# Kernel optimization log

Hardware: AMD Instinct MI355X
Metric: run time of the kernel (lower is better)

Reference implementation:

```python
import jax, jax.numpy as jnp
import numpy as np
import math

NEG = -9e15
NOISE_SCALE = 0.4

def _gat(h, A, a0, a1, a2, a3):
    # e_k[b,i,j] = leakyrelu(sum_d h[b,i,d]*h[b,j,d]*a_k[d])  (== (h[i]*h[j]) @ a_k)
    def score(a):
        return jax.nn.leaky_relu(jnp.einsum('bid,bjd->bij', h * a, h), 0.2)
    e0, e1, e2, e3 = score(a0), score(a1), score(a2), score(a3)
    alpha = jnp.where(A == 1, e0, NEG)
    alpha = jnp.where(A == 2, e1, alpha)
    alpha = jnp.where(A == 3, e2, alpha)
    alpha = jnp.where(A == 4, e3, alpha)
    alpha = jax.nn.softmax(alpha, axis=-1)
    return jnp.einsum('bij,bjd->bid', alpha, h)

def _ave_pooling(h, mask):
    length = jnp.sum(mask, axis=1)                      # [B]
    return jnp.sum(h * mask[:, :, None], axis=1) / length[:, None]

def _att_pooling(h, star, mask):
    sim = jnp.exp(jnp.einsum('bnd,bd->bn', h, star))    # [B,N]
    sim = sim * mask
    sim = sim / (jnp.sum(sim, axis=-1, keepdims=True) + 1e-24)
    return jnp.sum(sim[:, :, None] * h, axis=1)         # [B,D]

def _forward(A, hidden, graph_mask, a0, a1, a2, a3, noise):
    step, D = noise.shape[0], hidden.shape[-1]
    star = _ave_pooling(hidden, graph_mask)
    embs = []
    for i in range(step):
        hidden = _gat(hidden, A, a0, a1, a2, a3)
        sim = jnp.einsum('bnd,bd->bn', hidden, star) / math.sqrt(D)
        alpha = jax.nn.sigmoid(sim)[:, :, None]
        hidden = (1.0 - alpha) * hidden + alpha * star[:, None, :]
        n = noise[i]
        n = n / jnp.maximum(jnp.linalg.norm(n, axis=-1, keepdims=True), 1e-12)
        hidden = hidden + jnp.sign(hidden) * n * NOISE_SCALE
        star = _att_pooling(hidden, star, graph_mask)
        embs.append(hidden)
    embeddings_cl = jnp.mean(jnp.stack(embs, axis=1), axis=1)
    return hidden, star, embeddings_cl

def setup_inputs() -> dict:
    key = jax.random.key(0)
    ks = jax.random.split(key, 8)
    B, N, D, STEP = 256, 128, 512, 3
    A = jax.random.randint(ks[0], (B, N, N), 0, 5, dtype=jnp.int64)
    hidden = jax.random.normal(ks[1], (B, N, D), dtype=jnp.float32)
    graph_mask = jnp.ones((B, N), dtype=jnp.float32)
    a0 = jax.random.normal(ks[2], (D,), dtype=jnp.float32) * 0.1
    a1 = jax.random.normal(ks[3], (D,), dtype=jnp.float32) * 0.1
    a2 = jax.random.normal(ks[4], (D,), dtype=jnp.float32) * 0.1
    a3 = jax.random.normal(ks[5], (D,), dtype=jnp.float32) * 0.1
    noise = jax.random.uniform(ks[6], (STEP, B, N, D), dtype=jnp.float32)
    return {"A": A, "hidden": hidden, "graph_mask": graph_mask,
            "a0": a0, "a1": a1, "a2": a2, "a3": a3, "noise": noise}

def reference(A, hidden, graph_mask, a0, a1, a2, a3, noise):
    return _forward(A, hidden, graph_mask, a0, a1, a2, a3, noise)
```

## Files before the change

kernel.cpp:

```cpp
#include <hip/hip_runtime.h>
#include <math.h>

#define BB 256
#define NN 128
#define DD 512
#define NEGV (-9e15f)

__global__ __launch_bounds__(256) void k_avepool(const float* __restrict__ h,
                                                 const float* __restrict__ mask,
                                                 float* __restrict__ star) {
    const int b = blockIdx.x;
    const int t = threadIdx.x;
    const float* hb = h + (size_t)b * NN * DD;
    const float* mb = mask + (size_t)b * NN;
    float acc0 = 0.f, acc1 = 0.f, L = 0.f;
    for (int n = 0; n < NN; ++n) {
        float m = mb[n];
        L += m;
        acc0 += m * hb[n * DD + t];
        acc1 += m * hb[n * DD + t + 256];
    }
    star[b * DD + t] = acc0 / L;
    star[b * DD + t + 256] = acc1 / L;
}

__global__ __launch_bounds__(1024, 1) void k_gat(const float* __restrict__ h_in,
                                                 const int* __restrict__ A,
                                                 const float* __restrict__ a0,
                                                 const float* __restrict__ a1,
                                                 const float* __restrict__ a2,
                                                 const float* __restrict__ a3,
                                                 float* __restrict__ h_gat) {
    __shared__ float4 hA[NN * 17];
    __shared__ float4 hB[NN * 17];
    __shared__ float  eselS[NN * 132];

    const int tid = threadIdx.x;
    const int b = blockIdx.x;
    const float* __restrict__ hb = h_in + (size_t)b * NN * DD;

    const bool fullJob = tid < 512;
    const bool quarterJob = (tid >= 512) && (tid < 768);
    int jjb = 0, jr = 0;
    if (fullJob) {
        int rem = tid;
        for (int k = 0; k < 16; ++k) {
            int c = 4 * k + 4;
            if (rem < c) { jjb = k; jr = rem; break; }
            rem -= c;
        }
    }
    const int i0 = jr * 2, i1 = i0 + 1;
    const int jb8 = jjb * 8;
    const int swi = (jr >> 2) & 7;
    const int swj = jjb & 7;
    const int qi = tid - 512;
    const int qrow = 64 + (qi >> 2);
    const int qj0 = 120 + 2 * (qi & 3);
    const int qswi = (qrow >> 3) & 7;

    auto stageAll = [&](float4* buf, int d0) {
        #pragma unroll
        for (int q = 0; q < 2; ++q) {
            int l = q * 1024 + tid;
            int row = l >> 4, c4 = l & 15;
            buf[row * 17 + (c4 ^ ((row >> 3) & 7))] = *(const float4*)(hb + row * DD + d0 + c4 * 4);
        }
    };

    float acc0[8][4], acc1[8][4];
    #pragma unroll
    for (int jj = 0; jj < 8; ++jj)
        #pragma unroll
        for (int k = 0; k < 4; ++k) { acc0[jj][k] = 0.f; acc1[jj][k] = 0.f; }

    stageAll(hA, 0);
    __syncthreads();
    for (int ck = 0; ck < 8; ++ck) {
        const int d0 = ck * 64;
        const float4* cur = (ck & 1) ? hB : hA;
        float4* nxt = (ck & 1) ? hA : hB;
        if (ck < 7) stageAll(nxt, d0 + 64);
        if (fullJob) {
            #pragma unroll 2
            for (int c4 = 0; c4 < 16; ++c4) {
                const int dbase = d0 + c4 * 4;
                const float av0x = a0[dbase],     av0y = a1[dbase],     av0z = a2[dbase],     av0w = a3[dbase];
                const float av1x = a0[dbase + 1], av1y = a1[dbase + 1], av1z = a2[dbase + 1], av1w = a3[dbase + 1];
                const float av2x = a0[dbase + 2], av2y = a1[dbase + 2], av2z = a2[dbase + 2], av2w = a3[dbase + 2];
                const float av3x = a0[dbase + 3], av3y = a1[dbase + 3], av3z = a2[dbase + 3], av3w = a3[dbase + 3];
                float4 hi0 = cur[i0 * 17 + (c4 ^ swi)];
                float4 hi1 = cur[i1 * 17 + (c4 ^ swi)];
                #pragma unroll
                for (int jj = 0; jj < 8; ++jj) {
                    float4 hj = cur[(jb8 + jj) * 17 + (c4 ^ swj)];
                    float p;
                    p = hi0.x * hj.x; acc0[jj][0] += p * av0x; acc0[jj][1] += p * av0y; acc0[jj][2] += p * av0z; acc0[jj][3] += p * av0w;
                    p = hi0.y * hj.y; acc0[jj][0] += p * av1x; acc0[jj][1] += p * av1y; acc0[jj][2] += p * av1z; acc0[jj][3] += p * av1w;
                    p = hi0.z * hj.z; acc0[jj][0] += p * av2x; acc0[jj][1] += p * av2y; acc0[jj][2] += p * av2z; acc0[jj][3] += p * av2w;
                    p = hi0.w * hj.w; acc0[jj][0] += p * av3x; acc0[jj][1] += p * av3y; acc0[jj][2] += p * av3z; acc0[jj][3] += p * av3w;
                    p = hi1.x * hj.x; acc1[jj][0] += p * av0x; acc1[jj][1] += p * av0y; acc1[jj][2] += p * av0z; acc1[jj][3] += p * av0w;
                    p = hi1.y * hj.y; acc1[jj][0] += p * av1x; acc1[jj][1] += p * av1y; acc1[jj][2] += p * av1z; acc1[jj][3] += p * av1w;
                    p = hi1.z * hj.z; acc1[jj][0] += p * av2x; acc1[jj][1] += p * av2y; acc1[jj][2] += p * av2z; acc1[jj][3] += p * av2w;
                    p = hi1.w * hj.w; acc1[jj][0] += p * av3x; acc1[jj][1] += p * av3y; acc1[jj][2] += p * av3z; acc1[jj][3] += p * av3w;
                }
            }
        } else if (quarterJob) {
            #pragma unroll 2
            for (int c4 = 0; c4 < 16; ++c4) {
                const int dbase = d0 + c4 * 4;
                const float av0x = a0[dbase],     av0y = a1[dbase],     av0z = a2[dbase],     av0w = a3[dbase];
                const float av1x = a0[dbase + 1], av1y = a1[dbase + 1], av1z = a2[dbase + 1], av1w = a3[dbase + 1];
                const float av2x = a0[dbase + 2], av2y = a1[dbase + 2], av2z = a2[dbase + 2], av2w = a3[dbase + 2];
                const float av3x = a0[dbase + 3], av3y = a1[dbase + 3], av3z = a2[dbase + 3], av3w = a3[dbase + 3];
                float4 hi0 = cur[qrow * 17 + (c4 ^ qswi)];
                #pragma unroll
                for (int jj = 0; jj < 2; ++jj) {
                    float4 hj = cur[(qj0 + jj) * 17 + (c4 ^ 7)];
                    float p;
                    p = hi0.x * hj.x; acc0[jj][0] += p * av0x; acc0[jj][1] += p * av0y; acc0[jj][2] += p * av0z; acc0[jj][3] += p * av0w;
                    p = hi0.y * hj.y; acc0[jj][0] += p * av1x; acc0[jj][1] += p * av1y; acc0[jj][2] += p * av1z; acc0[jj][3] += p * av1w;
                    p = hi0.z * hj.z; acc0[jj][0] += p * av2x; acc0[jj][1] += p * av2y; acc0[jj][2] += p * av2z; acc0[jj][3] += p * av2w;
                    p = hi0.w * hj.w; acc0[jj][0] += p * av3x; acc0[jj][1] += p * av3y; acc0[jj][2] += p * av3z; acc0[jj][3] += p * av3w;
                }
            }
        }
        __syncthreads();
    }

    {
        auto selv = [](const float* a4, int Av) -> float {
            float e = (Av == 1) ? a4[0] : (Av == 2) ? a4[1] : (Av == 3) ? a4[2] : a4[3];
            float lr = (e > 0.f) ? e : 0.2f * e;
            return (Av >= 1 && Av <= 4) ? lr : NEGV;
        };
        const int* __restrict__ Ab = A + (size_t)b * NN * NN;
        if (fullJob) {
            #pragma unroll
            for (int jj = 0; jj < 8; ++jj) {
                const int j = jb8 + jj;
                int Av;
                Av = Ab[i0 * NN + j];  eselS[i0 * 132 + j] = selv(acc0[jj], Av);
                Av = Ab[i1 * NN + j];  eselS[i1 * 132 + j] = selv(acc1[jj], Av);
                Av = Ab[j * NN + i0];  eselS[j * 132 + i0] = selv(acc0[jj], Av);
                Av = Ab[j * NN + i1];  eselS[j * 132 + i1] = selv(acc1[jj], Av);
            }
        } else if (quarterJob) {
            #pragma unroll
            for (int jj = 0; jj < 2; ++jj) {
                const int j = qj0 + jj;
                int Av;
                Av = Ab[qrow * NN + j];  eselS[qrow * 132 + j] = selv(acc0[jj], Av);
                Av = Ab[j * NN + qrow];  eselS[j * 132 + qrow] = selv(acc0[jj], Av);
            }
        }
        __syncthreads();
    }

    {
        const int it4 = tid >> 8;
        const int sub = tid & 255;
        const int ti = sub >> 4, tj = sub & 15;
        const int li0 = it4 * 32 + ti * 2, li1 = li0 + 1;
        float s0[8], s1[8];
        #pragma unroll
        for (int jj = 0; jj < 8; ++jj) {
            s0[jj] = eselS[li0 * 132 + tj + 16 * jj];
            s1[jj] = eselS[li1 * 132 + tj + 16 * jj];
        }
        float m0 = s0[0], m1 = s1[0];
        #pragma unroll
        for (int jj = 1; jj < 8; ++jj) { m0 = fmaxf(m0, s0[jj]); m1 = fmaxf(m1, s1[jj]); }
        #pragma unroll
        for (int off = 1; off < 16; off <<= 1) {
            m0 = fmaxf(m0, __shfl_xor(m0, off));
            m1 = fmaxf(m1, __shfl_xor(m1, off));
        }
        float e0[8], e1[8], sum0 = 0.f, sum1 = 0.f;
        #pragma unroll
        for (int jj = 0; jj < 8; ++jj) {
            e0[jj] = expf(s0[jj] - m0); sum0 += e0[jj];
            e1[jj] = expf(s1[jj] - m1); sum1 += e1[jj];
        }
        #pragma unroll
        for (int off = 1; off < 16; off <<= 1) {
            sum0 += __shfl_xor(sum0, off);
            sum1 += __shfl_xor(sum1, off);
        }
        #pragma unroll
        for (int jj = 0; jj < 8; ++jj) {
            eselS[li0 * 132 + tj + 16 * jj] = e0[jj] / sum0;
            eselS[li1 * 132 + tj + 16 * jj] = e1[jj] / sum1;
        }
    }
    __syncthreads();

    stageAll(hA, 0);
    __syncthreads();
    const int gd = tid & 15, jh = (tid >> 4) & 1, rsub = (tid >> 5) & 1, wv = tid >> 6;
    const int rbase = wv * 16 + rsub;
    const int jbase = jh * 64;
#define PVROW(r, ac) { s[r].x += (ac) * hv.x; s[r].y += (ac) * hv.y; s[r].z += (ac) * hv.z; s[r].w += (ac) * hv.w; }
    for (int ck = 0; ck < 8; ++ck) {
        const int d0 = ck * 64;
        const float4* cur = (ck & 1) ? hB : hA;
        float4* nxt = (ck & 1) ? hA : hB;
        if (tid >= 512) {
            if (ck < 7) {
                #pragma unroll
                for (int q = 0; q < 4; ++q) {
                    int l = q * 512 + (tid - 512);
                    int row = l >> 4, c4 = l & 15;
                    nxt[row * 17 + (c4 ^ ((row >> 3) & 7))] = *(const float4*)(hb + row * DD + d0 + 64 + c4 * 4);
                }
            }
        } else {
            float4 s[8];
            #pragma unroll
            for (int r = 0; r < 8; ++r) s[r] = make_float4(0.f, 0.f, 0.f, 0.f);
            #pragma unroll 2
            for (int jq = 0; jq < 16; ++jq) {
                const int j0 = jbase + jq * 4;
                const int swz = (j0 >> 3) & 7;
                float4 av0 = *(const float4*)(&eselS[(rbase +  0) * 132 + j0]);
                float4 av1 = *(const float4*)(&eselS[(rbase +  2) * 132 + j0]);
                float4 av2 = *(const float4*)(&eselS[(rbase +  4) * 132 + j0]);
                float4 av3 = *(const float4*)(&eselS[(rbase +  6) * 132 + j0]);
                float4 av4 = *(const float4*)(&eselS[(rbase +  8) * 132 + j0]);
                float4 av5 = *(const float4*)(&eselS[(rbase + 10) * 132 + j0]);
                float4 av6 = *(const float4*)(&eselS[(rbase + 12) * 132 + j0]);
                float4 av7 = *(const float4*)(&eselS[(rbase + 14) * 132 + j0]);
                float4 hv;
                hv = cur[(j0 + 0) * 17 + (gd ^ swz)];
                PVROW(0, av0.x) PVROW(1, av1.x) PVROW(2, av2.x) PVROW(3, av3.x)
                PVROW(4, av4.x) PVROW(5, av5.x) PVROW(6, av6.x) PVROW(7, av7.x)
                hv = cur[(j0 + 1) * 17 + (gd ^ swz)];
                PVROW(0, av0.y) PVROW(1, av1.y) PVROW(2, av2.y) PVROW(3, av3.y)
                PVROW(4, av4.y) PVROW(5, av5.y) PVROW(6, av6.y) PVROW(7, av7.y)
                hv = cur[(j0 + 2) * 17 + (gd ^ swz)];
                PVROW(0, av0.z) PVROW(1, av1.z) PVROW(2, av2.z) PVROW(3, av3.z)
                PVROW(4, av4.z) PVROW(5, av5.z) PVROW(6, av6.z) PVROW(7, av7.z)
                hv = cur[(j0 + 3) * 17 + (gd ^ swz)];
                PVROW(0, av0.w) PVROW(1, av1.w) PVROW(2, av2.w) PVROW(3, av3.w)
                PVROW(4, av4.w) PVROW(5, av5.w) PVROW(6, av6.w) PVROW(7, av7.w)
            }
            #pragma unroll
            for (int r = 0; r < 8; ++r) {
                float mx = __shfl_xor(s[r].x, 16);
                float my = __shfl_xor(s[r].y, 16);
                float mz = __shfl_xor(s[r].z, 16);
                float mw = __shfl_xor(s[r].w, 16);
                s[r].x += mx; s[r].y += my; s[r].z += mz; s[r].w += mw;
            }
            if (jh == 0) {
                float* outp = h_gat + ((size_t)b * NN + rbase) * DD + d0 + gd * 4;
                #pragma unroll
                for (int r = 0; r < 8; ++r) *(float4*)(outp + (size_t)(2 * r) * DD) = s[r];
            }
        }
        __syncthreads();
    }
#undef PVROW
}

__global__ __launch_bounds__(256) void k_mix(const float* __restrict__ h_gat,
                                             const float* __restrict__ star,
                                             const float* __restrict__ noise_s,
                                             const float* __restrict__ h1p,
                                             const float* __restrict__ h2p,
                                             float* __restrict__ h_out,
                                             float* __restrict__ embs,
                                             float* __restrict__ sims,
                                             int mode) {
    const int b = blockIdx.y;
    const int tid = threadIdx.x;
    const int wave = tid >> 6, lane = tid & 63;
    const int row0 = blockIdx.x * 16 + wave * 4;
    const float* stp = star + (size_t)b * DD + lane * 8;
    float4 st0 = *(const float4*)(stp);
    float4 st1 = *(const float4*)(stp + 4);
    const float inv3 = 1.0f / 3.0f;

    for (int rr = 0; rr < 4; ++rr) {
        const int row = row0 + rr;
        const size_t base = ((size_t)b * NN + row) * DD + lane * 8;
        float4 hg0 = *(const float4*)(h_gat + base);
        float4 hg1 = *(const float4*)(h_gat + base + 4);
        float4 n0 = *(const float4*)(noise_s + base);
        float4 n1 = *(const float4*)(noise_s + base + 4);
        float dot = hg0.x*st0.x + hg0.y*st0.y + hg0.z*st0.z + hg0.w*st0.w
                  + hg1.x*st1.x + hg1.y*st1.y + hg1.z*st1.z + hg1.w*st1.w;
        float nn = n0.x*n0.x + n0.y*n0.y + n0.z*n0.z + n0.w*n0.w
                 + n1.x*n1.x + n1.y*n1.y + n1.z*n1.z + n1.w*n1.w;
        #pragma unroll
        for (int off = 1; off < 64; off <<= 1) {
            dot += __shfl_xor(dot, off);
            nn  += __shfl_xor(nn, off);
        }
        const float sim = dot / 22.62741699796952f;
        const float al = 1.0f / (1.0f + expf(-sim));
        const float ns = 0.4f / fmaxf(sqrtf(nn), 1e-12f);

        float hm, sg, hn[8];
        float hgv[8] = {hg0.x,hg0.y,hg0.z,hg0.w,hg1.x,hg1.y,hg1.z,hg1.w};
        float stv[8] = {st0.x,st0.y,st0.z,st0.w,st1.x,st1.y,st1.z,st1.w};
        float nv [8] = {n0.x,n0.y,n0.z,n0.w,n1.x,n1.y,n1.z,n1.w};
        #pragma unroll
        for (int c = 0; c < 8; ++c) {
            hm = (1.0f - al) * hgv[c] + al * stv[c];
            sg = (hm > 0.f) ? 1.f : ((hm < 0.f) ? -1.f : 0.f);
            hn[c] = hm + sg * nv[c] * ns;
        }
        *(float4*)(h_out + base)     = make_float4(hn[0], hn[1], hn[2], hn[3]);
        *(float4*)(h_out + base + 4) = make_float4(hn[4], hn[5], hn[6], hn[7]);

        float d2 = hn[0]*stv[0] + hn[1]*stv[1] + hn[2]*stv[2] + hn[3]*stv[3]
                 + hn[4]*stv[4] + hn[5]*stv[5] + hn[6]*stv[6] + hn[7]*stv[7];
        #pragma unroll
        for (int off = 1; off < 64; off <<= 1) d2 += __shfl_xor(d2, off);
        if (lane == 0) sims[b * NN + row] = d2;

        if (mode == 1) {
            float4 a0v = *(const float4*)(h1p + base);
            float4 a1v = *(const float4*)(h1p + base + 4);
            float4 b0v = *(const float4*)(h2p + base);
            float4 b1v = *(const float4*)(h2p + base + 4);
            float h1v[8] = {a0v.x,a0v.y,a0v.z,a0v.w,a1v.x,a1v.y,a1v.z,a1v.w};
            float h2v[8] = {b0v.x,b0v.y,b0v.z,b0v.w,b1v.x,b1v.y,b1v.z,b1v.w};
            float ev[8];
            #pragma unroll
            for (int c = 0; c < 8; ++c) {
                float e = h1v[c] * inv3;
                e += h2v[c] * inv3;
                e += hn[c] * inv3;
                ev[c] = e;
            }
            *(float4*)(embs + base)     = make_float4(ev[0], ev[1], ev[2], ev[3]);
            *(float4*)(embs + base + 4) = make_float4(ev[4], ev[5], ev[6], ev[7]);
        } else if (mode == 2) {
            *(float4*)(embs + base)     = make_float4(hn[0]*inv3, hn[1]*inv3, hn[2]*inv3, hn[3]*inv3);
            *(float4*)(embs + base + 4) = make_float4(hn[4]*inv3, hn[5]*inv3, hn[6]*inv3, hn[7]*inv3);
        } else if (mode == 3) {
            float4 ea = *(const float4*)(embs + base);
            float4 eb = *(const float4*)(embs + base + 4);
            ea.x += hn[0]*inv3; ea.y += hn[1]*inv3; ea.z += hn[2]*inv3; ea.w += hn[3]*inv3;
            eb.x += hn[4]*inv3; eb.y += hn[5]*inv3; eb.z += hn[6]*inv3; eb.w += hn[7]*inv3;
            *(float4*)(embs + base)     = ea;
            *(float4*)(embs + base + 4) = eb;
        }
    }
}

__global__ __launch_bounds__(256) void k_attpool2(const float* __restrict__ h,
                                                  const float* __restrict__ sims,
                                                  const float* __restrict__ mask,
                                                  float* __restrict__ star_out) {
    __shared__ float simS[NN];
    __shared__ float wS[NN];
    __shared__ float sh_M, sh_inv;
    const int b = blockIdx.x;
    const int tid = threadIdx.x;
    if (tid < NN) simS[tid] = sims[b * NN + tid];
    __syncthreads();
    if (tid < 64) {
        float v = fmaxf(simS[tid], simS[tid + 64]);
        #pragma unroll
        for (int off = 1; off < 64; off <<= 1) v = fmaxf(v, __shfl_xor(v, off));
        if (tid == 0) sh_M = v;
    }
    __syncthreads();
    const float M = sh_M;
    if (tid < NN) wS[tid] = expf(simS[tid] - M) * mask[b * NN + tid];
    __syncthreads();
    if (tid < 64) {
        float v = wS[tid] + wS[tid + 64];
        #pragma unroll
        for (int off = 1; off < 64; off <<= 1) v += __shfl_xor(v, off);
        if (tid == 0) sh_inv = 1.0f / (v + 1e-24f * expf(-M));
    }
    __syncthreads();
    const float inv = sh_inv;
    const float* hb = h + (size_t)b * NN * DD;
    float acc0 = 0.f, acc1 = 0.f;
    for (int n = 0; n < NN; ++n) {
        const float w = wS[n];
        acc0 += w * hb[n * DD + tid];
        acc1 += w * hb[n * DD + tid + 256];
    }
    star_out[b * DD + tid] = acc0 * inv;
    star_out[b * DD + tid + 256] = acc1 * inv;
}

extern "C" void kernel_launch(void* const* d_in, const int* in_sizes, int n_in,
                              void* d_out, int out_size, void* d_ws, size_t ws_size,
                              hipStream_t stream) {
    const int*   A      = (const int*)d_in[0];
    const float* hidden = (const float*)d_in[1];
    const float* mask   = (const float*)d_in[2];
    const float* a0     = (const float*)d_in[3];
    const float* a1     = (const float*)d_in[4];
    const float* a2     = (const float*)d_in[5];
    const float* a3     = (const float*)d_in[6];
    const float* noise  = (const float*)d_in[7];

    float* out_h    = (float*)d_out;
    float* out_star = out_h + (size_t)BB * NN * DD;
    float* out_embs = out_star + (size_t)BB * DD;

    const size_t hElems = (size_t)BB * NN * DD;
    const size_t simsElems = (size_t)BB * NN;
    const size_t needDeferred = (2 * hElems + (size_t)BB * DD + simsElems) * sizeof(float);
    const bool deferred = ws_size >= needDeferred;

    float* ws_h1   = (float*)d_ws;
    float* ws_h2   = deferred ? (ws_h1 + hElems) : ws_h1;
    float* ws_star = (deferred ? ws_h2 : ws_h1) + hElems;
    float* ws_sims = ws_star + (size_t)BB * DD;

    k_avepool<<<BB, 256, 0, stream>>>(hidden, mask, ws_star);

    for (int s = 0; s < 3; ++s) {
        const float* hin = (s == 0) ? hidden : (deferred ? ((s == 1) ? ws_h1 : ws_h2) : ws_h1);
        k_gat<<<BB, 1024, 0, stream>>>(hin, A, a0, a1, a2, a3, out_h);

        const float* ns = noise + (size_t)s * BB * NN * DD;
        float* hout = (s == 2) ? out_h : (deferred ? ((s == 0) ? ws_h1 : ws_h2) : ws_h1);
        float* sout = (s == 2) ? out_star : ws_star;
        int mode;
        const float* h1p = nullptr; const float* h2p = nullptr;
        if (deferred) {
            if (s < 2) mode = 0;
            else { mode = 1; h1p = ws_h1; h2p = ws_h2; }
        } else {
            mode = (s == 0) ? 2 : 3;
        }
        k_mix<<<dim3(8, BB), 256, 0, stream>>>(out_h, ws_star, ns, h1p, h2p,
                                               hout, out_embs, ws_sims, mode);
        k_attpool2<<<BB, 256, 0, stream>>>(hout, ws_sims, mask, sout);
    }
}
```

Baseline: 780.8 us.

## Fuse attention pooling into next GAT kernel and change LDS swizzle

Splits attention pooling into a small weight-calculation kernel (softmax weights and inverse normaliser) and moves the weighted sum over nodes into the idle threads (768-831) of the next GAT kernel. Those threads read the already-staged hidden chunks in shared memory, so the separate pass that re-read the full hidden tensor from global memory is gone. The LDS XOR swizzle now uses (row>>1)&7 instead of (row>>3)&7, to change bank-conflict behaviour on the staged float4 tiles. The cost is extra kernel launches and heavier per-block work in the GAT kernel, which runs at one block per CU.

Result: slower. 819.8 us (+5.0%).

```diff
diff --git a/kernel.cpp b/kernel.cpp
--- a/kernel.cpp
+++ b/kernel.cpp
@@ -30,14 +30,25 @@
                                                  const float* __restrict__ a1,
                                                  const float* __restrict__ a2,
                                                  const float* __restrict__ a3,
-                                                 float* __restrict__ h_gat) {
+                                                 float* __restrict__ h_gat,
+                                                 const float* __restrict__ wG,
+                                                 const float* __restrict__ invG,
+                                                 float* __restrict__ star_prev,
+                                                 int doAtt) {
     __shared__ float4 hA[NN * 17];
     __shared__ float4 hB[NN * 17];
     __shared__ float  eselS[NN * 132];
+    __shared__ float  wLDS[NN];
+    __shared__ float  invSh;
 
     const int tid = threadIdx.x;
     const int b = blockIdx.x;
     const float* __restrict__ hb = h_in + (size_t)b * NN * DD;
+
+    if (doAtt) {
+        if (tid < NN) wLDS[tid] = wG[b * NN + tid];
+        if (tid == 128) invSh = invG[b];
+    }
 
     const bool fullJob = tid < 512;
     const bool quarterJob = (tid >= 512) && (tid < 768);
@@ -52,19 +63,18 @@
     }
     const int i0 = jr * 2, i1 = i0 + 1;
     const int jb8 = jjb * 8;
-    const int swi = (jr >> 2) & 7;
-    const int swj = jjb & 7;
+    const int swi = jr & 7;
     const int qi = tid - 512;
     const int qrow = 64 + (qi >> 2);
     const int qj0 = 120 + 2 * (qi & 3);
-    const int qswi = (qrow >> 3) & 7;
+    const int qswi = (qrow >> 1) & 7;
 
     auto stageAll = [&](float4* buf, int d0) {
         #pragma unroll
         for (int q = 0; q < 2; ++q) {
             int l = q * 1024 + tid;
             int row = l >> 4, c4 = l & 15;
-            buf[row * 17 + (c4 ^ ((row >> 3) & 7))] = *(const float4*)(hb + row * DD + d0 + c4 * 4);
+            buf[row * 17 + (c4 ^ ((row >> 1) & 7))] = *(const float4*)(hb + row * DD + d0 + c4 * 4);
         }
     };
 
@@ -93,7 +103,8 @@
                 float4 hi1 = cur[i1 * 17 + (c4 ^ swi)];
                 #pragma unroll
                 for (int jj = 0; jj < 8; ++jj) {
-                    float4 hj = cur[(jb8 + jj) * 17 + (c4 ^ swj)];
+                    const int jrow = jb8 + jj;
+                    float4 hj = cur[jrow * 17 + (c4 ^ ((jrow >> 1) & 7))];
                     float p;
                     p = hi0.x * hj.x; acc0[jj][0] += p * av0x; acc0[jj][1] += p * av0y; acc0[jj][2] += p * av0z; acc0[jj][3] += p * av0w;
                     p = hi0.y * hj.y; acc0[jj][0] += p * av1x; acc0[jj][1] += p * av1y; acc0[jj][2] += p * av1z; acc0[jj][3] += p * av1w;
@@ -116,7 +127,8 @@
                 float4 hi0 = cur[qrow * 17 + (c4 ^ qswi)];
                 #pragma unroll
                 for (int jj = 0; jj < 2; ++jj) {
-                    float4 hj = cur[(qj0 + jj) * 17 + (c4 ^ 7)];
+                    const int jrow = qj0 + jj;
+                    float4 hj = cur[jrow * 17 + (c4 ^ ((jrow >> 1) & 7))];
                     float p;
                     p = hi0.x * hj.x; acc0[jj][0] += p * av0x; acc0[jj][1] += p * av0y; acc0[jj][2] += p * av0z; acc0[jj][3] += p * av0w;
                     p = hi0.y * hj.y; acc0[jj][0] += p * av1x; acc0[jj][1] += p * av1y; acc0[jj][2] += p * av1z; acc0[jj][3] += p * av1w;
@@ -124,6 +136,14 @@
                     p = hi0.w * hj.w; acc0[jj][0] += p * av3x; acc0[jj][1] += p * av3y; acc0[jj][2] += p * av3z; acc0[jj][3] += p * av3w;
                 }
             }
+        } else if (doAtt && tid >= 768 && tid < 832) {
+            const int dl = tid - 768;
+            const int c4 = dl >> 2, comp = dl & 3;
+            const float* curF = (const float*)cur;
+            float acc = 0.f;
+            for (int n = 0; n < NN; ++n)
+                acc += wLDS[n] * curF[(n * 17 + (c4 ^ ((n >> 1) & 7))) * 4 + comp];
+            star_prev[b * DD + d0 + dl] = acc * invSh;
         }
         __syncthreads();
     }
@@ -211,7 +231,7 @@
                 for (int q = 0; q < 4; ++q) {
                     int l = q * 512 + (tid - 512);
                     int row = l >> 4, c4 = l & 15;
-                    nxt[row * 17 + (c4 ^ ((row >> 3) & 7))] = *(const float4*)(hb + row * DD + d0 + 64 + c4 * 4);
+                    nxt[row * 17 + (c4 ^ ((row >> 1) & 7))] = *(const float4*)(hb + row * DD + d0 + 64 + c4 * 4);
                 }
             }
         } else {
@@ -221,7 +241,6 @@
             #pragma unroll 2
             for (int jq = 0; jq < 16; ++jq) {
                 const int j0 = jbase + jq * 4;
-                const int swz = (j0 >> 3) & 7;
                 float4 av0 = *(const float4*)(&eselS[(rbase +  0) * 132 + j0]);
                 float4 av1 = *(const float4*)(&eselS[(rbase +  2) * 132 + j0]);
                 float4 av2 = *(const float4*)(&eselS[(rbase +  4) * 132 + j0]);
@@ -231,16 +250,16 @@
                 float4 av6 = *(const float4*)(&eselS[(rbase + 12) * 132 + j0]);
                 float4 av7 = *(const float4*)(&eselS[(rbase + 14) * 132 + j0]);
                 float4 hv;
-                hv = cur[(j0 + 0) * 17 + (gd ^ swz)];
+                hv = cur[(j0 + 0) * 17 + (gd ^ (((j0 + 0) >> 1) & 7))];
                 PVROW(0, av0.x) PVROW(1, av1.x) PVROW(2, av2.x) PVROW(3, av3.x)
                 PVROW(4, av4.x) PVROW(5, av5.x) PVROW(6, av6.x) PVROW(7, av7.x)
-                hv = cur[(j0 + 1) * 17 + (gd ^ swz)];
+                hv = cur[(j0 + 1) * 17 + (gd ^ (((j0 + 1) >> 1) & 7))];
                 PVROW(0, av0.y) PVROW(1, av1.y) PVROW(2, av2.y) PVROW(3, av3.y)
                 PVROW(4, av4.y) PVROW(5, av5.y) PVROW(6, av6.y) PVROW(7, av7.y)
-                hv = cur[(j0 + 2) * 17 + (gd ^ swz)];
+                hv = cur[(j0 + 2) * 17 + (gd ^ (((j0 + 2) >> 1) & 7))];
                 PVROW(0, av0.z) PVROW(1, av1.z) PVROW(2, av2.z) PVROW(3, av3.z)
                 PVROW(4, av4.z) PVROW(5, av5.z) PVROW(6, av6.z) PVROW(7, av7.z)
-                hv = cur[(j0 + 3) * 17 + (gd ^ swz)];
+                hv = cur[(j0 + 3) * 17 + (gd ^ (((j0 + 3) >> 1) & 7))];
                 PVROW(0, av0.w) PVROW(1, av1.w) PVROW(2, av2.w) PVROW(3, av3.w)
                 PVROW(4, av4.w) PVROW(5, av5.w) PVROW(6, av6.w) PVROW(7, av7.w)
             }
@@ -351,6 +370,37 @@
     }
 }
 
+__global__ __launch_bounds__(128) void k_wcalc(const float* __restrict__ sims,
+                                               const float* __restrict__ mask,
+                                               float* __restrict__ wG,
+                                               float* __restrict__ invG) {
+    __shared__ float simS[NN];
+    __shared__ float wSsh[NN];
+    __shared__ float sh_M;
+    const int b = blockIdx.x;
+    const int tid = threadIdx.x;
+    simS[tid] = sims[b * NN + tid];
+    __syncthreads();
+    if (tid < 64) {
+        float v = fmaxf(simS[tid], simS[tid + 64]);
+        #pragma unroll
+        for (int off = 1; off < 64; off <<= 1) v = fmaxf(v, __shfl_xor(v, off));
+        if (tid == 0) sh_M = v;
+    }
+    __syncthreads();
+    const float M = sh_M;
+    float wv = expf(simS[tid] - M) * mask[b * NN + tid];
+    wSsh[tid] = wv;
+    wG[b * NN + tid] = wv;
+    __syncthreads();
+    if (tid < 64) {
+        float v = wSsh[tid] + wSsh[tid + 64];
+        #pragma unroll
+        for (int off = 1; off < 64; off <<= 1) v += __shfl_xor(v, off);
+        if (tid == 0) invG[b] = 1.0f / (v + 1e-24f * expf(-M));
+    }
+}
+
 __global__ __launch_bounds__(256) void k_attpool2(const float* __restrict__ h,
                                                   const float* __restrict__ sims,
                                                   const float* __restrict__ mask,
@@ -408,34 +458,51 @@
     float* out_embs = out_star + (size_t)BB * DD;
 
     const size_t hElems = (size_t)BB * NN * DD;
-    const size_t simsElems = (size_t)BB * NN;
-    const size_t needDeferred = (2 * hElems + (size_t)BB * DD + simsElems) * sizeof(float);
+    const size_t sElems = (size_t)BB * DD;
+    const size_t nElems = (size_t)BB * NN;
+    const size_t needDeferred = (2 * hElems + 2 * sElems + 2 * nElems + BB) * sizeof(float);
     const bool deferred = ws_size >= needDeferred;
 
-    float* ws_h1   = (float*)d_ws;
-    float* ws_h2   = deferred ? (ws_h1 + hElems) : ws_h1;
-    float* ws_star = (deferred ? ws_h2 : ws_h1) + hElems;
-    float* ws_sims = ws_star + (size_t)BB * DD;
-
-    k_avepool<<<BB, 256, 0, stream>>>(hidden, mask, ws_star);
-
-    for (int s = 0; s < 3; ++s) {
-        const float* hin = (s == 0) ? hidden : (deferred ? ((s == 1) ? ws_h1 : ws_h2) : ws_h1);
-        k_gat<<<BB, 1024, 0, stream>>>(hin, A, a0, a1, a2, a3, out_h);
-
-        const float* ns = noise + (size_t)s * BB * NN * DD;
-        float* hout = (s == 2) ? out_h : (deferred ? ((s == 0) ? ws_h1 : ws_h2) : ws_h1);
-        float* sout = (s == 2) ? out_star : ws_star;
-        int mode;
-        const float* h1p = nullptr; const float* h2p = nullptr;
-        if (deferred) {
-            if (s < 2) mode = 0;
-            else { mode = 1; h1p = ws_h1; h2p = ws_h2; }
-        } else {
-            mode = (s == 0) ? 2 : 3;
-        }
-        k_mix<<<dim3(8, BB), 256, 0, stream>>>(out_h, ws_star, ns, h1p, h2p,
-                                               hout, out_embs, ws_sims, mode);
-        k_attpool2<<<BB, 256, 0, stream>>>(hout, ws_sims, mask, sout);
+    float* ws_h1 = (float*)d_ws;
+    if (deferred) {
+        float* ws_h2      = ws_h1 + hElems;
+        float* ws_starPre = ws_h2 + hElems;
+        float* ws_starA   = ws_starPre + sElems;
+        float* ws_sims    = ws_starA + sElems;
+        float* ws_wG      = ws_sims + nElems;
+        float* ws_invG    = ws_wG + nElems;
+
+        k_avepool<<<BB, 256, 0, stream>>>(hidden, mask, ws_starPre);
+
+        k_gat<<<BB, 1024, 0, stream>>>(hidden, A, a0, a1, a2, a3, out_h,
+                                       nullptr, nullptr, nullptr, 0);
+        k_mix<<<dim3(8, BB), 256, 0, stream>>>(out_h, ws_starPre, noise, nullptr, nullptr,
+                                               ws_h1, out_embs, ws_sims, 0);
+        k_wcalc<<<BB, 128, 0, stream>>>(ws_sims, mask, ws_wG, ws_invG);
+        k_gat<<<BB, 1024, 0, stream>>>(ws_h1, A, a0, a1, a2, a3, out_h,
+                                       ws_wG, ws_invG, ws_starA, 1);
+        k_mix<<<dim3(8, BB), 256, 0, stream>>>(out_h, ws_starA, noise + hElems, nullptr, nullptr,
+                                               ws_h2, out_embs, ws_sims, 0);
+        k_wcalc<<<BB, 128, 0, stream>>>(ws_sims, mask, ws_wG, ws_invG);
+        k_gat<<<BB, 1024, 0, stream>>>(ws_h2, A, a0, a1, a2, a3, out_h,
+                                       ws_wG, ws_invG, ws_starA, 1);
+        k_mix<<<dim3(8, BB), 256, 0, stream>>>(out_h, ws_starA, noise + 2 * hElems, ws_h1, ws_h2,
+                                               out_h, out_embs, ws_sims, 1);
+        k_attpool2<<<BB, 256, 0, stream>>>(out_h, ws_sims, mask, out_star);
+    } else {
+        float* ws_star = ws_h1 + hElems;
+        float* ws_sims = ws_star + sElems;
+        k_avepool<<<BB, 256, 0, stream>>>(hidden, mask, ws_star);
+        for (int s = 0; s < 3; ++s) {
+            const float* hin = (s == 0) ? hidden : ws_h1;
+            k_gat<<<BB, 1024, 0, stream>>>(hin, A, a0, a1, a2, a3, out_h,
+                                           nullptr, nullptr, nullptr, 0);
+            const float* ns = noise + (size_t)s * hElems;
+            float* hout = (s == 2) ? out_h : ws_h1;
+            float* sout = (s == 2) ? out_star : ws_star;
+            k_mix<<<dim3(8, BB), 256, 0, stream>>>(out_h, ws_star, ns, nullptr, nullptr,
+                                                   hout, out_embs, ws_sims, (s == 0) ? 2 : 3);
+            k_attpool2<<<BB, 256, 0, stream>>>(hout, ws_sims, mask, sout);
+        }
     }
 }
```

## Split fused GAT kernel into separate score and PV kernels via global scratch

Applied to the files above, without the earlier changes.

The single 1024-thread-per-batch GAT kernel is replaced by two kernels, each launched as 2 blocks of 512 threads per batch. The first computes the masked attention scores and writes them to global memory, reusing the out_embs buffer as scratch. The second does the softmax for 64 rows and multiplies by h. This aims to raise occupancy and parallelism, at the cost of an extra global write and read of the score matrix, duplicated h staging across blocks, and no double buffering in the PV stage. Reusing out_embs as scratch only works if embeddings are written after the last PV kernel, as in the deferred path.

Result: slower. 955.3 us (+22.3%).

```diff
diff --git a/kernel.cpp b/kernel.cpp
--- a/kernel.cpp
+++ b/kernel.cpp
@@ -24,26 +24,24 @@
     star[b * DD + t + 256] = acc1 / L;
 }
 
-__global__ __launch_bounds__(1024, 1) void k_gat(const float* __restrict__ h_in,
-                                                 const int* __restrict__ A,
-                                                 const float* __restrict__ a0,
-                                                 const float* __restrict__ a1,
-                                                 const float* __restrict__ a2,
-                                                 const float* __restrict__ a3,
-                                                 float* __restrict__ h_gat) {
+__global__ __launch_bounds__(512, 2) void k_score(const float* __restrict__ h_in,
+                                                  const int* __restrict__ A,
+                                                  const float* __restrict__ a0,
+                                                  const float* __restrict__ a1,
+                                                  const float* __restrict__ a2,
+                                                  const float* __restrict__ a3,
+                                                  float* __restrict__ esel_g) {
     __shared__ float4 hA[NN * 17];
     __shared__ float4 hB[NN * 17];
-    __shared__ float  eselS[NN * 132];
 
     const int tid = threadIdx.x;
-    const int b = blockIdx.x;
+    const int bx = blockIdx.x, b = blockIdx.y;
     const float* __restrict__ hb = h_in + (size_t)b * NN * DD;
 
-    const bool fullJob = tid < 512;
-    const bool quarterJob = (tid >= 512) && (tid < 768);
+    const bool fullJob = tid < 256;
     int jjb = 0, jr = 0;
-    if (fullJob) {
-        int rem = tid;
+    {
+        int rem = bx * 256 + (tid & 255);
         for (int k = 0; k < 16; ++k) {
             int c = 4 * k + 4;
             if (rem < c) { jjb = k; jr = rem; break; }
@@ -54,15 +52,16 @@
     const int jb8 = jjb * 8;
     const int swi = (jr >> 2) & 7;
     const int swj = jjb & 7;
-    const int qi = tid - 512;
+    const bool quarterJob = (bx == 1) && (tid >= 256);
+    const int qi = tid - 256;
     const int qrow = 64 + (qi >> 2);
     const int qj0 = 120 + 2 * (qi & 3);
     const int qswi = (qrow >> 3) & 7;
 
     auto stageAll = [&](float4* buf, int d0) {
         #pragma unroll
-        for (int q = 0; q < 2; ++q) {
-            int l = q * 1024 + tid;
+        for (int q = 0; q < 4; ++q) {
+            int l = q * 512 + tid;
             int row = l >> 4, c4 = l & 15;
             buf[row * 17 + (c4 ^ ((row >> 3) & 7))] = *(const float4*)(hb + row * DD + d0 + c4 * 4);
         }
@@ -135,38 +134,51 @@
             return (Av >= 1 && Av <= 4) ? lr : NEGV;
         };
         const int* __restrict__ Ab = A + (size_t)b * NN * NN;
+        float* __restrict__ eb = esel_g + (size_t)b * NN * NN;
         if (fullJob) {
             #pragma unroll
             for (int jj = 0; jj < 8; ++jj) {
                 const int j = jb8 + jj;
                 int Av;
-                Av = Ab[i0 * NN + j];  eselS[i0 * 132 + j] = selv(acc0[jj], Av);
-                Av = Ab[i1 * NN + j];  eselS[i1 * 132 + j] = selv(acc1[jj], Av);
-                Av = Ab[j * NN + i0];  eselS[j * 132 + i0] = selv(acc0[jj], Av);
-                Av = Ab[j * NN + i1];  eselS[j * 132 + i1] = selv(acc1[jj], Av);
+                Av = Ab[i0 * NN + j];  eb[i0 * NN + j] = selv(acc0[jj], Av);
+                Av = Ab[i1 * NN + j];  eb[i1 * NN + j] = selv(acc1[jj], Av);
+                Av = Ab[j * NN + i0];  eb[j * NN + i0] = selv(acc0[jj], Av);
+                Av = Ab[j * NN + i1];  eb[j * NN + i1] = selv(acc1[jj], Av);
             }
         } else if (quarterJob) {
             #pragma unroll
             for (int jj = 0; jj < 2; ++jj) {
                 const int j = qj0 + jj;
                 int Av;
-                Av = Ab[qrow * NN + j];  eselS[qrow * 132 + j] = selv(acc0[jj], Av);
-                Av = Ab[j * NN + qrow];  eselS[j * 132 + qrow] = selv(acc0[jj], Av);
+                Av = Ab[qrow * NN + j];  eb[qrow * NN + j] = selv(acc0[jj], Av);
+                Av = Ab[j * NN + qrow];  eb[j * NN + qrow] = selv(acc0[jj], Av);
             }
         }
-        __syncthreads();
-    }
+    }
+}
+
+__global__ __launch_bounds__(512, 2) void k_pv(const float* __restrict__ h_in,
+                                               const float* __restrict__ esel_g,
+                                               float* __restrict__ h_gat) {
+    __shared__ float4 hA[NN * 17];
+    __shared__ float  alphaS[64 * 132];
+
+    const int tid = threadIdx.x;
+    const int bx = blockIdx.x, b = blockIdx.y;
+    const int r0 = bx * 64;
+    const float* __restrict__ hb = h_in + (size_t)b * NN * DD;
 
     {
-        const int it4 = tid >> 8;
+        const int it2 = tid >> 8;
         const int sub = tid & 255;
         const int ti = sub >> 4, tj = sub & 15;
-        const int li0 = it4 * 32 + ti * 2, li1 = li0 + 1;
+        const int li0 = r0 + it2 * 32 + ti * 2, li1 = li0 + 1;
+        const float* __restrict__ eb = esel_g + (size_t)b * NN * NN;
         float s0[8], s1[8];
         #pragma unroll
         for (int jj = 0; jj < 8; ++jj) {
-            s0[jj] = eselS[li0 * 132 + tj + 16 * jj];
-            s1[jj] = eselS[li1 * 132 + tj + 16 * jj];
+            s0[jj] = eb[li0 * NN + tj + 16 * jj];
+            s1[jj] = eb[li1 * NN + tj + 16 * jj];
         }
         float m0 = s0[0], m1 = s1[0];
         #pragma unroll
@@ -189,74 +201,57 @@
         }
         #pragma unroll
         for (int jj = 0; jj < 8; ++jj) {
-            eselS[li0 * 132 + tj + 16 * jj] = e0[jj] / sum0;
-            eselS[li1 * 132 + tj + 16 * jj] = e1[jj] / sum1;
-        }
-    }
-    __syncthreads();
-
-    stageAll(hA, 0);
-    __syncthreads();
+            alphaS[(li0 - r0) * 132 + tj + 16 * jj] = e0[jj] / sum0;
+            alphaS[(li1 - r0) * 132 + tj + 16 * jj] = e1[jj] / sum1;
+        }
+    }
+
     const int gd = tid & 15, jh = (tid >> 4) & 1, rsub = (tid >> 5) & 1, wv = tid >> 6;
-    const int rbase = wv * 16 + rsub;
+    const int rloc = wv * 8 + rsub;
     const int jbase = jh * 64;
 #define PVROW(r, ac) { s[r].x += (ac) * hv.x; s[r].y += (ac) * hv.y; s[r].z += (ac) * hv.z; s[r].w += (ac) * hv.w; }
     for (int ck = 0; ck < 8; ++ck) {
         const int d0 = ck * 64;
-        const float4* cur = (ck & 1) ? hB : hA;
-        float4* nxt = (ck & 1) ? hA : hB;
-        if (tid >= 512) {
-            if (ck < 7) {
-                #pragma unroll
-                for (int q = 0; q < 4; ++q) {
-                    int l = q * 512 + (tid - 512);
-                    int row = l >> 4, c4 = l & 15;
-                    nxt[row * 17 + (c4 ^ ((row >> 3) & 7))] = *(const float4*)(hb + row * DD + d0 + 64 + c4 * 4);
-                }
-            }
-        } else {
-            float4 s[8];
+        #pragma unroll
+        for (int q = 0; q < 4; ++q) {
+            int l = q * 512 + tid;
+            int row = l >> 4, c4 = l & 15;
+            hA[row * 17 + (c4 ^ ((row >> 3) & 7))] = *(const float4*)(hb + row * DD + d0 + c4 * 4);
+        }
+        __syncthreads();
+        float4 s[4];
+        #pragma unroll
+        for (int r = 0; r < 4; ++r) s[r] = make_float4(0.f, 0.f, 0.f, 0.f);
+        #pragma unroll 2
+        for (int jq = 0; jq < 16; ++jq) {
+            const int j0 = jbase + jq * 4;
+            const int swz = (j0 >> 3) & 7;
+            float4 av0 = *(const float4*)(&alphaS[(rloc + 0) * 132 + j0]);
+            float4 av1 = *(const float4*)(&alphaS[(rloc + 2) * 132 + j0]);
+            float4 av2 = *(const float4*)(&alphaS[(rloc + 4) * 132 + j0]);
+            float4 av3 = *(const float4*)(&alphaS[(rloc + 6) * 132 + j0]);
+            float4 hv;
+            hv = hA[(j0 + 0) * 17 + (gd ^ swz)];
+            PVROW(0, av0.x) PVROW(1, av1.x) PVROW(2, av2.x) PVROW(3, av3.x)
+            hv = hA[(j0 + 1) * 17 + (gd ^ swz)];
+            PVROW(0, av0.y) PVROW(1, av1.y) PVROW(2, av2.y) PVROW(3, av3.y)
+            hv = hA[(j0 + 2) * 17 + (gd ^ swz)];
+            PVROW(0, av0.z) PVROW(1, av1.z) PVROW(2, av2.z) PVROW(3, av3.z)
+            hv = hA[(j0 + 3) * 17 + (gd ^ swz)];
+            PVROW(0, av0.w) PVROW(1, av1.w) PVROW(2, av2.w) PVROW(3, av3.w)
+        }
+        #pragma unroll
+        for (int r = 0; r < 4; ++r) {
+            float mx = __shfl_xor(s[r].x, 16);
+            float my = __shfl_xor(s[r].y, 16);
+            float mz = __shfl_xor(s[r].z, 16);
+            float mw = __shfl_xor(s[r].w, 16);
+            s[r].x += mx; s[r].y += my; s[r].z += mz; s[r].w += mw;
+        }
+        if (jh == 0) {
+            float* outp = h_gat + ((size_t)b * NN + r0 + rloc) * DD + d0 + gd * 4;
             #pragma unroll
-            for (int r = 0; r < 8; ++r) s[r] = make_float4(0.f, 0.f, 0.f, 0.f);
-            #pragma unroll 2
-            for (int jq = 0; jq < 16; ++jq) {
-                const int j0 = jbase + jq * 4;
-                const int swz = (j0 >> 3) & 7;
-                float4 av0 = *(const float4*)(&eselS[(rbase +  0) * 132 + j0]);
-                float4 av1 = *(const float4*)(&eselS[(rbase +  2) * 132 + j0]);
-                float4 av2 = *(const float4*)(&eselS[(rbase +  4) * 132 + j0]);
-                float4 av3 = *(const float4*)(&eselS[(rbase +  6) * 132 + j0]);
-                float4 av4 = *(const float4*)(&eselS[(rbase +  8) * 132 + j0]);
-                float4 av5 = *(const float4*)(&eselS[(rbase + 10) * 132 + j0]);
-                float4 av6 = *(const float4*)(&eselS[(rbase + 12) * 132 + j0]);
-                float4 av7 = *(const float4*)(&eselS[(rbase + 14) * 132 + j0]);
-                float4 hv;
-                hv = cur[(j0 + 0) * 17 + (gd ^ swz)];
-                PVROW(0, av0.x) PVROW(1, av1.x) PVROW(2, av2.x) PVROW(3, av3.x)
-                PVROW(4, av4.x) PVROW(5, av5.x) PVROW(6, av6.x) PVROW(7, av7.x)
-                hv = cur[(j0 + 1) * 17 + (gd ^ swz)];
-                PVROW(0, av0.y) PVROW(1, av1.y) PVROW(2, av2.y) PVROW(3, av3.y)
-                PVROW(4, av4.y) PVROW(5, av5.y) PVROW(6, av6.y) PVROW(7, av7.y)
-                hv = cur[(j0 + 2) * 17 + (gd ^ swz)];
-                PVROW(0, av0.z) PVROW(1, av1.z) PVROW(2, av2.z) PVROW(3, av3.z)
-                PVROW(4, av4.z) PVROW(5, av5.z) PVROW(6, av6.z) PVROW(7, av7.z)
-                hv = cur[(j0 + 3) * 17 + (gd ^ swz)];
-                PVROW(0, av0.w) PVROW(1, av1.w) PVROW(2, av2.w) PVROW(3, av3.w)
-                PVROW(4, av4.w) PVROW(5, av5.w) PVROW(6, av6.w) PVROW(7, av7.w)
-            }
-            #pragma unroll
-            for (int r = 0; r < 8; ++r) {
-                float mx = __shfl_xor(s[r].x, 16);
-                float my = __shfl_xor(s[r].y, 16);
-                float mz = __shfl_xor(s[r].z, 16);
-                float mw = __shfl_xor(s[r].w, 16);
-                s[r].x += mx; s[r].y += my; s[r].z += mz; s[r].w += mw;
-            }
-            if (jh == 0) {
-                float* outp = h_gat + ((size_t)b * NN + rbase) * DD + d0 + gd * 4;
-                #pragma unroll
-                for (int r = 0; r < 8; ++r) *(float4*)(outp + (size_t)(2 * r) * DD) = s[r];
-            }
+            for (int r = 0; r < 4; ++r) *(float4*)(outp + (size_t)(2 * r) * DD) = s[r];
         }
         __syncthreads();
     }
@@ -416,12 +411,14 @@
     float* ws_h2   = deferred ? (ws_h1 + hElems) : ws_h1;
     float* ws_star = (deferred ? ws_h2 : ws_h1) + hElems;
     float* ws_sims = ws_star + (size_t)BB * DD;
+    float* g_esel  = out_embs;
 
     k_avepool<<<BB, 256, 0, stream>>>(hidden, mask, ws_star);
 
     for (int s = 0; s < 3; ++s) {
         const float* hin = (s == 0) ? hidden : (deferred ? ((s == 1) ? ws_h1 : ws_h2) : ws_h1);
-        k_gat<<<BB, 1024, 0, stream>>>(hin, A, a0, a1, a2, a3, out_h);
+        k_score<<<dim3(2, BB), 512, 0, stream>>>(hin, A, a0, a1, a2, a3, g_esel);
+        k_pv<<<dim3(2, BB), 512, 0, stream>>>(hin, g_esel, out_h);
 
         const float* ns = noise + (size_t)s * BB * NN * DD;
         float* hout = (s == 2) ? out_h : (deferred ? ((s == 0) ? ws_h1 : ws_h2) : ws_h1);
```
